# Optimization experiments

Measured on AMD Instinct MI355X. Metric: run time of the kernel, lower is better.

Reference implementation:

```python
import jax, jax.numpy as jnp
import numpy as np

N_NODES = 100000
N_EDGES = 6400000


def setup_inputs() -> dict:
    key = jax.random.key(0)
    k1, k2, k3 = jax.random.split(key, 3)
    x = jax.random.normal(k1, (N_NODES, 1), dtype=jnp.float32)
    edge_index = jax.random.randint(k2, (2, N_EDGES), 0, N_NODES, dtype=jnp.int64)
    edge_weight = jax.random.normal(k3, (N_EDGES,), dtype=jnp.float32)
    return {"x": x, "edge_index": edge_index, "edge_weight": edge_weight}


def reference(x, edge_index, edge_weight):
    # flow='target_to_source': messages come from x[edge_index[1]] and are
    # scatter-added into nodes edge_index[0].
    src = edge_index[0]  # aggregation target (flow reversed)
    dst = edge_index[1]  # message source
    msgs = edge_weight[:, None] * x[dst]  # [E, 1]
    out = jax.ops.segment_sum(msgs, src, num_segments=N_NODES)  # [N, 1]
    return out
```

## Files before the change

kernel.cpp:

```cpp
#include <hip/hip_runtime.h>

#define N_NODES 100000
#define N_EDGES 6400000
#define RANGES 4
#define RANGE_S 25000
#define NB 64
#define BLK 1024
#define FIX_SCALE 1048576.0f
#define FIX_INV   (1.0f / 1048576.0f)

#define TBLOCKS 256
#define TTHREADS 1024
#define EPB (N_EDGES / TBLOCKS)
#define GPB (EPB / 8)
#define HALF_S 50000
#define NP 2

__global__ void zero_out_kernel(float* __restrict__ out, int n) {
    int i = blockIdx.x * blockDim.x + threadIdx.x;
    if (i < n) out[i] = 0.0f;
}

__global__ void __launch_bounds__(256) scatter_direct_kernel(
        const float* __restrict__ x, const int* __restrict__ ei,
        const float* __restrict__ w, float* __restrict__ out) {
    int t = blockIdx.x * blockDim.x + threadIdx.x;
    int e0 = t * 4;
    if (e0 >= N_EDGES) return;
    int4   s4 = *reinterpret_cast<const int4*>(ei + e0);
    int4   d4 = *reinterpret_cast<const int4*>(ei + N_EDGES + e0);
    float4 w4 = *reinterpret_cast<const float4*>(w + e0);
    atomicAdd(&out[s4.x], w4.x * x[d4.x]);
    atomicAdd(&out[s4.y], w4.y * x[d4.y]);
    atomicAdd(&out[s4.z], w4.z * x[d4.z]);
    atomicAdd(&out[s4.w], w4.w * x[d4.w]);
}

__device__ __forceinline__ unsigned bf16_rne(float f) {
    unsigned b = __float_as_uint(f);
    b += 0x7FFFu + ((b >> 16) & 1u);
    return b >> 16;
}
__device__ __forceinline__ float bf16_to_f(unsigned h) {
    return __uint_as_float(h << 16);
}

__global__ void __launch_bounds__(TTHREADS, 4) transform_kernel(
        const float* __restrict__ x, const int* __restrict__ ei,
        const float* __restrict__ w, unsigned short* __restrict__ msg) {
    __shared__ unsigned short xh[HALF_S];
    const int tid  = threadIdx.x;
    const int base = blockIdx.x * EPB;
    const int* dstp = ei + N_EDGES;

    uint4 o[4];
    #pragma unroll
    for (int k = 0; k < 4; ++k) o[k] = make_uint4(0u, 0u, 0u, 0u);

    #pragma unroll
    for (int p = 0; p < NP; ++p) {
        if (p) __syncthreads();
        const float4* xs = reinterpret_cast<const float4*>(x + p * HALF_S);
        for (int j = tid; j < HALF_S / 8; j += TTHREADS) {
            float4 f0 = xs[j * 2], f1 = xs[j * 2 + 1];
            uint4 pk;
            pk.x = bf16_rne(f0.x) | (bf16_rne(f0.y) << 16);
            pk.y = bf16_rne(f0.z) | (bf16_rne(f0.w) << 16);
            pk.z = bf16_rne(f1.x) | (bf16_rne(f1.y) << 16);
            pk.w = bf16_rne(f1.z) | (bf16_rne(f1.w) << 16);
            *reinterpret_cast<uint4*>(&xh[j * 8]) = pk;
        }
        __syncthreads();
        const int lo = p * HALF_S;

        #pragma unroll
        for (int k = 0; k < 4; ++k) {
            int idx = k * TTHREADS + tid;
            if (idx < GPB) {
                int e0 = base + idx * 8;
                int4   da = *reinterpret_cast<const int4*>(dstp + e0);
                int4   db = *reinterpret_cast<const int4*>(dstp + e0 + 4);
                float4 wa = *reinterpret_cast<const float4*>(w + e0);
                float4 wb = *reinterpret_cast<const float4*>(w + e0 + 4);

                unsigned a0 = (unsigned)(da.x - lo), a1 = (unsigned)(da.y - lo),
                         a2 = (unsigned)(da.z - lo), a3 = (unsigned)(da.w - lo),
                         a4 = (unsigned)(db.x - lo), a5 = (unsigned)(db.y - lo),
                         a6 = (unsigned)(db.z - lo), a7 = (unsigned)(db.w - lo);
                float v0 = bf16_to_f(xh[a0 < HALF_S ? a0 : 0u]);
                float v1 = bf16_to_f(xh[a1 < HALF_S ? a1 : 0u]);
                float v2 = bf16_to_f(xh[a2 < HALF_S ? a2 : 0u]);
                float v3 = bf16_to_f(xh[a3 < HALF_S ? a3 : 0u]);
                float v4 = bf16_to_f(xh[a4 < HALF_S ? a4 : 0u]);
                float v5 = bf16_to_f(xh[a5 < HALF_S ? a5 : 0u]);
                float v6 = bf16_to_f(xh[a6 < HALF_S ? a6 : 0u]);
                float v7 = bf16_to_f(xh[a7 < HALF_S ? a7 : 0u]);
                o[k].x |= (a0 < HALF_S ? bf16_rne(wa.x * v0)       : 0u)
                        | (a1 < HALF_S ? bf16_rne(wa.y * v1) << 16 : 0u);
                o[k].y |= (a2 < HALF_S ? bf16_rne(wa.z * v2)       : 0u)
                        | (a3 < HALF_S ? bf16_rne(wa.w * v3) << 16 : 0u);
                o[k].z |= (a4 < HALF_S ? bf16_rne(wb.x * v4)       : 0u)
                        | (a5 < HALF_S ? bf16_rne(wb.y * v5) << 16 : 0u);
                o[k].w |= (a6 < HALF_S ? bf16_rne(wb.z * v6)       : 0u)
                        | (a7 < HALF_S ? bf16_rne(wb.w * v7) << 16 : 0u);
            }
        }
    }

    #pragma unroll
    for (int k = 0; k < 4; ++k) {
        int idx = k * TTHREADS + tid;
        if (idx < GPB) {
            *reinterpret_cast<uint4*>(msg + base + idx * 8) = o[k];
        }
    }
}

__global__ void __launch_bounds__(BLK) bin_kernel(
        const int* __restrict__ ei, const unsigned short* __restrict__ msg,
        unsigned short* __restrict__ partial) {
    __shared__ int bins[RANGE_S];
    const int b    = blockIdx.x;
    const int xcd  = b & 7;
    const int slot = b >> 3;
    const int r    = slot & 3;
    const int c    = (slot >> 2) * 8 + xcd;

    for (int i = threadIdx.x; i < RANGE_S; i += BLK) bins[i] = 0;
    __syncthreads();

    const int chunk = N_EDGES / NB;
    const int base  = c * chunk;
    const int end   = base + chunk;
    const int lo    = r * RANGE_S;

    for (int e = base + (int)threadIdx.x * 8; e < end; e += BLK * 8) {
        int4 sa = *reinterpret_cast<const int4*>(ei + e);
        int4 sb = *reinterpret_cast<const int4*>(ei + e + 4);
        uint4 mm = *reinterpret_cast<const uint4*>(msg + e);

        unsigned a[8] = {(unsigned)(sa.x-lo),(unsigned)(sa.y-lo),(unsigned)(sa.z-lo),(unsigned)(sa.w-lo),
                         (unsigned)(sb.x-lo),(unsigned)(sb.y-lo),(unsigned)(sb.z-lo),(unsigned)(sb.w-lo)};
        float f[8] = {
            __uint_as_float((mm.x & 0xFFFFu) << 16), __uint_as_float(mm.x & 0xFFFF0000u),
            __uint_as_float((mm.y & 0xFFFFu) << 16), __uint_as_float(mm.y & 0xFFFF0000u),
            __uint_as_float((mm.z & 0xFFFFu) << 16), __uint_as_float(mm.z & 0xFFFF0000u),
            __uint_as_float((mm.w & 0xFFFFu) << 16), __uint_as_float(mm.w & 0xFFFF0000u)
        };
        int mi[8];
        #pragma unroll
        for (int k = 0; k < 8; ++k) mi[k] = (int)__builtin_rintf(f[k] * FIX_SCALE);
        #pragma unroll
        for (int k = 0; k < 8; ++k) {
            if (a[k] < RANGE_S) atomicAdd(&bins[a[k]], mi[k]);
        }
    }
    __syncthreads();

    unsigned short* outp = partial + (size_t)(r * NB + c) * RANGE_S;
    for (int i = threadIdx.x; i < RANGE_S / 4; i += BLK) {
        int4 v = *reinterpret_cast<const int4*>(&bins[i * 4]);
        uint2 pk;
        pk.x = bf16_rne((float)v.x * FIX_INV) | (bf16_rne((float)v.y * FIX_INV) << 16);
        pk.y = bf16_rne((float)v.z * FIX_INV) | (bf16_rne((float)v.w * FIX_INV) << 16);
        *reinterpret_cast<uint2*>(outp + i * 4) = pk;
    }
}

__global__ void reduce_range_kernel(const unsigned short* __restrict__ partial,
                                    float* __restrict__ out) {
    int i = blockIdx.x * blockDim.x + threadIdx.x;
    int n0 = i * 4;
    if (n0 >= N_NODES) return;
    int r = n0 / RANGE_S;
    int s = n0 - r * RANGE_S;
    const unsigned short* bp = partial + (size_t)(r * NB) * RANGE_S + s;
    float4 acc = make_float4(0.f, 0.f, 0.f, 0.f);
    for (int j = 0; j < NB; ++j) {
        uint2 v = *reinterpret_cast<const uint2*>(bp + (size_t)j * RANGE_S);
        acc.x += bf16_to_f(v.x & 0xFFFFu);
        acc.y += bf16_to_f(v.x >> 16);
        acc.z += bf16_to_f(v.y & 0xFFFFu);
        acc.w += bf16_to_f(v.y >> 16);
    }
    *reinterpret_cast<float4*>(out + n0) = acc;
}

extern "C" void kernel_launch(void* const* d_in, const int* in_sizes, int n_in,
                              void* d_out, int out_size, void* d_ws, size_t ws_size,
                              hipStream_t stream) {
    const float* x   = (const float*)d_in[0];
    const int*   ei  = (const int*)d_in[1];
    const float* w   = (const float*)d_in[2];
    float*       out = (float*)d_out;

    const size_t msg_bytes     = (size_t)N_EDGES * 2;
    const size_t partial_bytes = (size_t)RANGES * NB * RANGE_S * 2;

    if (ws_size >= msg_bytes + partial_bytes) {
        unsigned short* msg     = (unsigned short*)d_ws;
        unsigned short* partial = (unsigned short*)((char*)d_ws + msg_bytes);
        transform_kernel<<<TBLOCKS, TTHREADS, 0, stream>>>(x, ei, w, msg);
        bin_kernel<<<RANGES * NB, BLK, 0, stream>>>(ei, msg, partial);
        reduce_range_kernel<<<(N_NODES / 4 + 255) / 256, 256, 0, stream>>>(partial, out);
    } else {
        zero_out_kernel<<<(N_NODES + 255) / 256, 256, 0, stream>>>(out, N_NODES);
        scatter_direct_kernel<<<(N_EDGES / 4 + 255) / 256, 256, 0, stream>>>(x, ei, w, out);
    }
}
```

Baseline: 42.31 us.

## Stage 80k nodes of x in LDS once and gather the rest from global

The transform kernel previously staged x in two 50k-node halves of bf16 LDS, and it read the edge indices and weights twice, once per pass. It now stages the first 80000 nodes in a single 160KB LDS array, makes one pass over the edges, and loads the remaining 20% of node values directly from global memory (fp32, L2-resident). This drops the second fill, the second edge read and a barrier. In exchange it gives up occupancy, since 160KB of LDS allows only one 1024-thread block per CU, and it adds divergent global gathers.

```diff
diff --git a/kernel.cpp b/kernel.cpp
--- a/kernel.cpp
+++ b/kernel.cpp
@@ -13,8 +13,7 @@
 #define TTHREADS 1024
 #define EPB (N_EDGES / TBLOCKS)
 #define GPB (EPB / 8)
-#define HALF_S 50000
-#define NP 2
+#define LDSN 80000
 
 __global__ void zero_out_kernel(float* __restrict__ out, int n) {
     int i = blockIdx.x * blockDim.x + threadIdx.x;
@@ -48,70 +47,60 @@
 __global__ void __launch_bounds__(TTHREADS, 4) transform_kernel(
         const float* __restrict__ x, const int* __restrict__ ei,
         const float* __restrict__ w, unsigned short* __restrict__ msg) {
-    __shared__ unsigned short xh[HALF_S];
+    __shared__ unsigned short xh[LDSN];
     const int tid  = threadIdx.x;
     const int base = blockIdx.x * EPB;
     const int* dstp = ei + N_EDGES;
 
-    uint4 o[4];
-    #pragma unroll
-    for (int k = 0; k < 4; ++k) o[k] = make_uint4(0u, 0u, 0u, 0u);
-
-    #pragma unroll
-    for (int p = 0; p < NP; ++p) {
-        if (p) __syncthreads();
-        const float4* xs = reinterpret_cast<const float4*>(x + p * HALF_S);
-        for (int j = tid; j < HALF_S / 8; j += TTHREADS) {
-            float4 f0 = xs[j * 2], f1 = xs[j * 2 + 1];
-            uint4 pk;
-            pk.x = bf16_rne(f0.x) | (bf16_rne(f0.y) << 16);
-            pk.y = bf16_rne(f0.z) | (bf16_rne(f0.w) << 16);
-            pk.z = bf16_rne(f1.x) | (bf16_rne(f1.y) << 16);
-            pk.w = bf16_rne(f1.z) | (bf16_rne(f1.w) << 16);
-            *reinterpret_cast<uint4*>(&xh[j * 8]) = pk;
-        }
-        __syncthreads();
-        const int lo = p * HALF_S;
-
-        #pragma unroll
-        for (int k = 0; k < 4; ++k) {
-            int idx = k * TTHREADS + tid;
-            if (idx < GPB) {
-                int e0 = base + idx * 8;
-                int4   da = *reinterpret_cast<const int4*>(dstp + e0);
-                int4   db = *reinterpret_cast<const int4*>(dstp + e0 + 4);
-                float4 wa = *reinterpret_cast<const float4*>(w + e0);
-                float4 wb = *reinterpret_cast<const float4*>(w + e0 + 4);
-
-                unsigned a0 = (unsigned)(da.x - lo), a1 = (unsigned)(da.y - lo),
-                         a2 = (unsigned)(da.z - lo), a3 = (unsigned)(da.w - lo),
-                         a4 = (unsigned)(db.x - lo), a5 = (unsigned)(db.y - lo),
-                         a6 = (unsigned)(db.z - lo), a7 = (unsigned)(db.w - lo);
-                float v0 = bf16_to_f(xh[a0 < HALF_S ? a0 : 0u]);
-                float v1 = bf16_to_f(xh[a1 < HALF_S ? a1 : 0u]);
-                float v2 = bf16_to_f(xh[a2 < HALF_S ? a2 : 0u]);
-                float v3 = bf16_to_f(xh[a3 < HALF_S ? a3 : 0u]);
-                float v4 = bf16_to_f(xh[a4 < HALF_S ? a4 : 0u]);
-                float v5 = bf16_to_f(xh[a5 < HALF_S ? a5 : 0u]);
-                float v6 = bf16_to_f(xh[a6 < HALF_S ? a6 : 0u]);
-                float v7 = bf16_to_f(xh[a7 < HALF_S ? a7 : 0u]);
-                o[k].x |= (a0 < HALF_S ? bf16_rne(wa.x * v0)       : 0u)
-                        | (a1 < HALF_S ? bf16_rne(wa.y * v1) << 16 : 0u);
-                o[k].y |= (a2 < HALF_S ? bf16_rne(wa.z * v2)       : 0u)
-                        | (a3 < HALF_S ? bf16_rne(wa.w * v3) << 16 : 0u);
-                o[k].z |= (a4 < HALF_S ? bf16_rne(wb.x * v4)       : 0u)
-                        | (a5 < HALF_S ? bf16_rne(wb.y * v5) << 16 : 0u);
-                o[k].w |= (a6 < HALF_S ? bf16_rne(wb.z * v6)       : 0u)
-                        | (a7 < HALF_S ? bf16_rne(wb.w * v7) << 16 : 0u);
-            }
-        }
+    const float4* xs = reinterpret_cast<const float4*>(x);
+    for (int j = tid; j < LDSN / 8; j += TTHREADS) {
+        float4 f0 = xs[j * 2], f1 = xs[j * 2 + 1];
+        uint4 pk;
+        pk.x = bf16_rne(f0.x) | (bf16_rne(f0.y) << 16);
+        pk.y = bf16_rne(f0.z) | (bf16_rne(f0.w) << 16);
+        pk.z = bf16_rne(f1.x) | (bf16_rne(f1.y) << 16);
+        pk.w = bf16_rne(f1.z) | (bf16_rne(f1.w) << 16);
+        *reinterpret_cast<uint4*>(&xh[j * 8]) = pk;
     }
+    __syncthreads();
 
     #pragma unroll
     for (int k = 0; k < 4; ++k) {
         int idx = k * TTHREADS + tid;
         if (idx < GPB) {
-            *reinterpret_cast<uint4*>(msg + base + idx * 8) = o[k];
+            int e0 = base + idx * 8;
+            int4   da = *reinterpret_cast<const int4*>(dstp + e0);
+            int4   db = *reinterpret_cast<const int4*>(dstp + e0 + 4);
+            float4 wa = *reinterpret_cast<const float4*>(w + e0);
+            float4 wb = *reinterpret_cast<const float4*>(w + e0 + 4);
+
+            unsigned a0 = (unsigned)da.x, a1 = (unsigned)da.y,
+                     a2 = (unsigned)da.z, a3 = (unsigned)da.w,
+                     a4 = (unsigned)db.x, a5 = (unsigned)db.y,
+                     a6 = (unsigned)db.z, a7 = (unsigned)db.w;
+            float v0 = bf16_to_f(xh[a0 < LDSN ? a0 : 0u]);
+            float v1 = bf16_to_f(xh[a1 < LDSN ? a1 : 0u]);
+            float v2 = bf16_to_f(xh[a2 < LDSN ? a2 : 0u]);
+            float v3 = bf16_to_f(xh[a3 < LDSN ? a3 : 0u]);
+            float v4 = bf16_to_f(xh[a4 < LDSN ? a4 : 0u]);
+            float v5 = bf16_to_f(xh[a5 < LDSN ? a5 : 0u]);
+            float v6 = bf16_to_f(xh[a6 < LDSN ? a6 : 0u]);
+            float v7 = bf16_to_f(xh[a7 < LDSN ? a7 : 0u]);
+            if (a0 >= LDSN) v0 = x[a0];
+            if (a1 >= LDSN) v1 = x[a1];
+            if (a2 >= LDSN) v2 = x[a2];
+            if (a3 >= LDSN) v3 = x[a3];
+            if (a4 >= LDSN) v4 = x[a4];
+            if (a5 >= LDSN) v5 = x[a5];
+            if (a6 >= LDSN) v6 = x[a6];
+            if (a7 >= LDSN) v7 = x[a7];
+
+            uint4 o;
+            o.x = bf16_rne(wa.x * v0) | (bf16_rne(wa.y * v1) << 16);
+            o.y = bf16_rne(wa.z * v2) | (bf16_rne(wa.w * v3) << 16);
+            o.z = bf16_rne(wb.x * v4) | (bf16_rne(wb.y * v5) << 16);
+            o.w = bf16_rne(wb.z * v6) | (bf16_rne(wb.w * v7) << 16);
+            *reinterpret_cast<uint4*>(msg + e0) = o;
         }
     }
 }
```

Result: faster. 40.28 us (median of 2 runs) (-4.8%).
